# Kernel optimization log

Hardware: AMD Instinct MI355X
Metric: run time of the kernel (lower is better)

Reference implementation:

```python
import jax, jax.numpy as jnp
import numpy as np

B, S, P, L, SEQ, H = 16, 40, 512, 48, 2048, 1024


def setup_inputs() -> dict:
    rng = np.random.default_rng(0)
    # sentence lengths include the trailing separator token; tokens used per sentence = len - 1
    sentence_length = rng.integers(8, L + 1, size=(B, S)).astype(np.int32)
    passage_length = rng.integers(30, S + 1, size=(B,)).astype(np.int32)
    # valid pair ids must be < passage_length per example
    pairs_list = (rng.random((B, P, 2)) * passage_length[:, None, None]).astype(np.int32)
    pairs_num = rng.integers(256, P + 1, size=(B,)).astype(np.int32)
    key = jax.random.key(0)
    top_rep = jax.random.normal(key, (B, SEQ, H), dtype=jnp.float32)
    return {
        "sentence_length": jnp.asarray(sentence_length),
        "pairs_list": jnp.asarray(pairs_list),
        "passage_length": jnp.asarray(passage_length),
        "pairs_num": jnp.asarray(pairs_num),
        "max_sentence_length": L,
        "top_rep": top_rep,
    }


def reference(sentence_length, pairs_list, passage_length, pairs_num, max_sentence_length, top_rep):
    Bb, Ss = sentence_length.shape
    Pp = pairs_list.shape[1]
    Ll = int(max_sentence_length)
    seq = top_rep.shape[1]

    # tokens per sentence (sentence_length - 1), zeroed beyond passage_length
    sen_mask = jnp.arange(Ss)[None, :] < passage_length[:, None]          # [B,S]
    tok = jnp.where(sen_mask, sentence_length - 1, 0)                     # [B,S]
    # start offset of each sentence in top_rep (first token at index 1)
    starts = 1 + jnp.cumsum(tok, axis=1) - tok                            # [B,S] exclusive cumsum + 1

    t = jnp.arange(Ll)
    idx = jnp.clip(starts[:, :, None] + t[None, None, :], 0, seq - 1)     # [B,S,L]
    valid = t[None, None, :] < tok[:, :, None]                            # [B,S,L]
    sen_emb = top_rep[jnp.arange(Bb)[:, None, None], idx]                 # [B,S,L,H] gather
    sen_emb = jnp.where(valid[..., None], sen_emb, jnp.zeros((), top_rep.dtype))

    # pair cls = mean over concat(sent_i tokens, sent_j tokens) = (sum_i+sum_j)/(cnt_i+cnt_j)
    sent_sum = sen_emb.sum(axis=2)                                        # [B,S,H]
    cnt = tok.astype(top_rep.dtype)                                       # [B,S]

    p = jnp.clip(pairs_list, 0, Ss - 1)                                   # [B,P,2]
    s0 = jnp.take_along_axis(sent_sum, p[:, :, 0][:, :, None], axis=1)    # [B,P,H]
    s1 = jnp.take_along_axis(sent_sum, p[:, :, 1][:, :, None], axis=1)    # [B,P,H]
    c0 = jnp.take_along_axis(cnt, p[:, :, 0], axis=1)                     # [B,P]
    c1 = jnp.take_along_axis(cnt, p[:, :, 1], axis=1)
    denom = jnp.maximum(c0 + c1, 1.0)

    pair_mask = jnp.arange(Pp)[None, :] < pairs_num[:, None]              # [B,P]
    cls = jnp.where(pair_mask[..., None], (s0 + s1) / denom[..., None], 0.0)
    return sen_emb, cls[:, :, None, :]                                    # [B,S,L,H], [B,P,1,H]
```

## Files before the change

### kernel.cpp

```cpp
#include <hip/hip_runtime.h>
#include <hip/hip_bf16.h>

#define CB   16
#define CS   40
#define CP   512
#define CL   48
#define CSEQ 2048
#define CH   1024
#define H4     (CH / 4)
#define TCHUNK 8
#define NCHUNK (CL / TCHUNK)

typedef float fvec4 __attribute__((ext_vector_type(4)));

__global__ void __launch_bounds__(256)
gather_kernel(const float* __restrict__ top_rep,
              const int* __restrict__ sentence_length,
              const int* __restrict__ passage_length,
              float* __restrict__ sen_emb,
              float* __restrict__ partial) {
    const int blk   = blockIdx.x;
    const int chunk = blk % NCHUNK;
    const int bs    = blk / NCHUNK;
    const int b     = bs / CS;
    const int s     = bs - b * CS;
    const int h4    = threadIdx.x;
    const int lane  = threadIdx.x & 63;

    const int pl = passage_length[b];
    int tokl = 0;
    if (lane < CS && lane < pl) tokl = sentence_length[b * CS + lane] - 1;
    int x = tokl;
    #pragma unroll
    for (int off = 1; off < 64; off <<= 1) {
        int y = __shfl_up(x, off);
        if (lane >= off) x += y;
    }
    const int tok   = __shfl(tokl, s);
    const int start = 1 + __shfl(x, s) - tok;

    const fvec4* __restrict__ rep =
        reinterpret_cast<const fvec4*>(top_rep) + (size_t)b * CSEQ * H4;
    fvec4* __restrict__ out =
        reinterpret_cast<fvec4*>(sen_emb) +
        ((size_t)bs * CL + (size_t)chunk * TCHUNK) * H4;

    fvec4 acc = {0.f, 0.f, 0.f, 0.f};
    const int t0 = chunk * TCHUNK;

    #pragma unroll
    for (int i = 0; i < TCHUNK; ++i) {
        const int t = t0 + i;
        fvec4 v = {0.f, 0.f, 0.f, 0.f};
        if (t < tok) {
            int row = start + t;
            row = min(max(row, 0), CSEQ - 1);
            v = rep[(size_t)row * H4 + h4];
        }
        __builtin_nontemporal_store(v, &out[(size_t)i * H4 + h4]);
        acc += v;
    }

    reinterpret_cast<fvec4*>(partial)[(size_t)blk * H4 + h4] = acc;
}

__global__ void __launch_bounds__(256)
reduce_kernel(const float* __restrict__ partial,
              float* __restrict__ sent_sum) {
    const int bs = blockIdx.x;
    const int h4 = threadIdx.x;
    const fvec4* __restrict__ p =
        reinterpret_cast<const fvec4*>(partial) + (size_t)bs * NCHUNK * H4;
    fvec4 acc = p[h4];
    #pragma unroll
    for (int c = 1; c < NCHUNK; ++c) acc += p[(size_t)c * H4 + h4];
    reinterpret_cast<fvec4*>(sent_sum)[(size_t)bs * H4 + h4] = acc;
}

__global__ void __launch_bounds__(256)
cls_kernel(const int* __restrict__ pairs_list,
           const int* __restrict__ pairs_num,
           const int* __restrict__ sentence_length,
           const int* __restrict__ passage_length,
           const float* __restrict__ sent_sum,
           float* __restrict__ cls) {
    const int blk = blockIdx.x;
    const int b   = blk / CP;
    const int i   = blk - b * CP;
    const int h4  = threadIdx.x;

    fvec4 r = {0.f, 0.f, 0.f, 0.f};

    if (i < pairs_num[b]) {
        int p0 = pairs_list[(size_t)blk * 2 + 0];
        int p1 = pairs_list[(size_t)blk * 2 + 1];
        p0 = min(max(p0, 0), CS - 1);
        p1 = min(max(p1, 0), CS - 1);

        const int pl = passage_length[b];
        const float c0 = (p0 < pl) ? (float)(sentence_length[b * CS + p0] - 1) : 0.f;
        const float c1 = (p1 < pl) ? (float)(sentence_length[b * CS + p1] - 1) : 0.f;
        const float denom = fmaxf(c0 + c1, 1.0f);

        const fvec4* __restrict__ ss = reinterpret_cast<const fvec4*>(sent_sum);
        fvec4 a0 = ss[(size_t)(b * CS + p0) * H4 + h4];
        fvec4 a1 = ss[(size_t)(b * CS + p1) * H4 + h4];

        r = (a0 + a1) / denom;
    }

    __builtin_nontemporal_store(
        r, &reinterpret_cast<fvec4*>(cls)[(size_t)blk * H4 + h4]);
}

extern "C" void kernel_launch(void* const* d_in, const int* in_sizes, int n_in,
                              void* d_out, int out_size, void* d_ws, size_t ws_size,
                              hipStream_t stream) {
    const int*   sentence_length = (const int*)  d_in[0];
    const int*   pairs_list      = (const int*)  d_in[1];
    const int*   passage_length  = (const int*)  d_in[2];
    const int*   pairs_num       = (const int*)  d_in[3];
    const float* top_rep         = (const float*)d_in[5];

    float* out     = (float*)d_out;
    float* sen_emb = out;
    float* cls     = out + (size_t)CB * CS * CL * CH;

    float* partial  = (float*)d_ws;
    float* sent_sum = partial + (size_t)CB * CS * NCHUNK * CH;

    gather_kernel<<<CB * CS * NCHUNK, 256, 0, stream>>>(
        top_rep, sentence_length, passage_length, sen_emb, partial);

    reduce_kernel<<<CB * CS, 256, 0, stream>>>(partial, sent_sum);

    cls_kernel<<<CB * CP, 256, 0, stream>>>(
        pairs_list, pairs_num, sentence_length, passage_length, sent_sum, cls);
}
```

Before: 45.53 us.

## Fuse chunk reduction into gather kernel via shared memory with 1024-thread blocks

The gather kernel now processes a whole sentence per 1024-thread block, with four 256-thread chunks of 12 tokens each. Per-chunk partial sums are combined in shared memory, so the separate reduce kernel launch and its global round trip for partial sums go away. In exchange there are fewer, larger blocks (640 instead of 3840) and a block-wide barrier. That may lower the memory-level parallelism available for the gather.

```diff
diff --git a/kernel.cpp b/kernel.cpp
--- a/kernel.cpp
+++ b/kernel.cpp
@@ -7,24 +7,23 @@
 #define CL   48
 #define CSEQ 2048
 #define CH   1024
-#define H4     (CH / 4)
-#define TCHUNK 8
-#define NCHUNK (CL / TCHUNK)
+#define H4   (CH / 4)
+#define NCHUNK 4
+#define TPT  (CL / NCHUNK)
 
 typedef float fvec4 __attribute__((ext_vector_type(4)));
 
-__global__ void __launch_bounds__(256)
+__global__ void __launch_bounds__(1024)
 gather_kernel(const float* __restrict__ top_rep,
               const int* __restrict__ sentence_length,
               const int* __restrict__ passage_length,
               float* __restrict__ sen_emb,
-              float* __restrict__ partial) {
-    const int blk   = blockIdx.x;
-    const int chunk = blk % NCHUNK;
-    const int bs    = blk / NCHUNK;
+              float* __restrict__ sent_sum) {
+    const int bs    = blockIdx.x;
     const int b     = bs / CS;
     const int s     = bs - b * CS;
-    const int h4    = threadIdx.x;
+    const int h4    = threadIdx.x & 255;
+    const int chunk = threadIdx.x >> 8;
     const int lane  = threadIdx.x & 63;
 
     const int pl = passage_length[b];
@@ -43,13 +42,13 @@
         reinterpret_cast<const fvec4*>(top_rep) + (size_t)b * CSEQ * H4;
     fvec4* __restrict__ out =
         reinterpret_cast<fvec4*>(sen_emb) +
-        ((size_t)bs * CL + (size_t)chunk * TCHUNK) * H4;
+        ((size_t)bs * CL + (size_t)chunk * TPT) * H4;
 
     fvec4 acc = {0.f, 0.f, 0.f, 0.f};
-    const int t0 = chunk * TCHUNK;
+    const int t0 = chunk * TPT;
 
-    #pragma unroll
-    for (int i = 0; i < TCHUNK; ++i) {
+    #pragma unroll 4
+    for (int i = 0; i < TPT; ++i) {
         const int t = t0 + i;
         fvec4 v = {0.f, 0.f, 0.f, 0.f};
         if (t < tok) {
@@ -61,20 +60,15 @@
         acc += v;
     }
 
-    reinterpret_cast<fvec4*>(partial)[(size_t)blk * H4 + h4] = acc;
-}
-
-__global__ void __launch_bounds__(256)
-reduce_kernel(const float* __restrict__ partial,
-              float* __restrict__ sent_sum) {
-    const int bs = blockIdx.x;
-    const int h4 = threadIdx.x;
-    const fvec4* __restrict__ p =
-        reinterpret_cast<const fvec4*>(partial) + (size_t)bs * NCHUNK * H4;
-    fvec4 acc = p[h4];
-    #pragma unroll
-    for (int c = 1; c < NCHUNK; ++c) acc += p[(size_t)c * H4 + h4];
-    reinterpret_cast<fvec4*>(sent_sum)[(size_t)bs * H4 + h4] = acc;
+    __shared__ fvec4 red[NCHUNK - 1][256];
+    if (chunk > 0) red[chunk - 1][h4] = acc;
+    __syncthreads();
+    if (chunk == 0) {
+        acc += red[0][h4];
+        acc += red[1][h4];
+        acc += red[2][h4];
+        reinterpret_cast<fvec4*>(sent_sum)[(size_t)bs * H4 + h4] = acc;
+    }
 }
 
 __global__ void __launch_bounds__(256)
@@ -126,13 +120,10 @@
     float* sen_emb = out;
     float* cls     = out + (size_t)CB * CS * CL * CH;
 
-    float* partial  = (float*)d_ws;
-    float* sent_sum = partial + (size_t)CB * CS * NCHUNK * CH;
+    float* sent_sum = (float*)d_ws;
 
-    gather_kernel<<<CB * CS * NCHUNK, 256, 0, stream>>>(
-        top_rep, sentence_length, passage_length, sen_emb, partial);
-
-    reduce_kernel<<<CB * CS, 256, 0, stream>>>(partial, sent_sum);
+    gather_kernel<<<CB * CS, 1024, 0, stream>>>(
+        top_rep, sentence_length, passage_length, sen_emb, sent_sum);
 
     cls_kernel<<<CB * CP, 256, 0, stream>>>(
         pairs_list, pairs_num, sentence_length, passage_length, sent_sum, cls);
```

New measurement: 42.47 us. 6.7% less time.
